# Performance work log

Hardware: AMD Instinct MI355X
Metric: run time of the kernel (lower is better)

The kernel has to match this reference:

```python
import jax, jax.numpy as jnp
import numpy as np

B, Q, K, H = 32, 256, 256, 128

def setup_inputs() -> dict:
    key = jax.random.key(0)
    k1, k2, k3, k4 = jax.random.split(key, 4)
    queries = jax.random.normal(k1, (B, Q, H), dtype=jnp.float32)
    keys = jax.random.normal(k2, (B, K, H), dtype=jnp.float32)
    values = jax.random.normal(k3, (B, K, H), dtype=jnp.float32)
    # nn.Linear(hidden_size, 1, bias=False) weight, stored as a length-H vector
    w = jax.random.normal(k4, (H,), dtype=jnp.float32) * (1.0 / np.sqrt(H))
    return {"queries": queries, "keys": keys, "values": values, "w": w}


def reference(queries, keys, values, w):
    # Y: [B, Q, K, H] broadcast sum, then tanh
    Y = jnp.tanh(queries[:, :, None, :] + keys[:, None, :, :])
    # scores: [B, Q, K] = Y @ w
    scores = jnp.einsum("bqkh,h->bqk", Y, w)
    attn = jax.nn.softmax(scores, axis=-1)
    # output: [B, Q, Hv]
    return jnp.einsum("bqk,bkv->bqv", attn, values)
```

## Files before the change

kernel.cpp:

```cpp
#include <hip/hip_runtime.h>
#include <math.h>

#define C2 2.8853900817779268f

typedef __attribute__((address_space(3))) unsigned int       lds_u32;
typedef const __attribute__((address_space(1))) unsigned int g_u32;

__device__ __forceinline__ void stage16(const float* g, float* l) {
    __builtin_amdgcn_global_load_lds((g_u32*)g, (lds_u32*)l, 16, 0, 0);
}

__global__ __launch_bounds__(512) void addattn_prep(const float* __restrict__ k_g,
                                                    float* __restrict__ ekt)
{
    int tid = blockIdx.x * 512 + threadIdx.x;
    int b   = tid >> 13;
    int r   = tid & 8191;
    int g   = r >> 8;
    int k   = r & 255;
    float4 kv = *(const float4*)(k_g + ((size_t)(b * 256 + k)) * 128 + (g << 2));
    float4 E;
    E.x = __builtin_amdgcn_exp2f(C2 * kv.x);
    E.y = __builtin_amdgcn_exp2f(C2 * kv.y);
    E.z = __builtin_amdgcn_exp2f(C2 * kv.z);
    E.w = __builtin_amdgcn_exp2f(C2 * kv.w);
    *(float4*)(ekt + (size_t)b * 32768 + ((k >> 6) << 13) + (g << 8) + ((k & 63) << 2)) = E;
}

__global__ __launch_bounds__(512) void addattn_kernel(
    const float* __restrict__ q_g, const float* __restrict__ ekt,
    const float* __restrict__ v_g, const float* __restrict__ w_g,
    float* __restrict__ out)
{
    __shared__ float kbuf[32768];
    __shared__ float eqst[4096];
    __shared__ float wlds[128];

    const int tid  = threadIdx.x;
    const int lane = tid & 63;
    const int wv   = __builtin_amdgcn_readfirstlane(tid >> 6);

    const int xcd = blockIdx.x & 7;
    const int sub = blockIdx.x >> 3;
    const int rg  = sub & 7;
    const int b   = (xcd << 2) + (sub >> 3);
    const int qr0 = (rg << 5) + (wv << 2);

    if (tid < 32) ((float4*)wlds)[tid] = ((const float4*)w_g)[tid];

    {
        const float* qb = q_g + (size_t)(b * 256 + qr0) * 128;
        #pragma unroll
        for (int j = 0; j < 2; ++j) {
            int f = lane + (j << 6);
            int r = f >> 5, c = f & 31;
            float4 qv = *(const float4*)(qb + (r << 7) + (c << 2));
            float4 E;
            E.x = __builtin_amdgcn_exp2f(C2 * qv.x);
            E.y = __builtin_amdgcn_exp2f(C2 * qv.y);
            E.z = __builtin_amdgcn_exp2f(C2 * qv.z);
            E.w = __builtin_amdgcn_exp2f(C2 * qv.w);
            *(float4*)&eqst[(wv << 9) + (r << 7) + (c << 2)] = E;
        }
    }

    {
        const float* ekb = ekt + (size_t)b * 32768;
        #pragma unroll
        for (int c = 0; c < 16; ++c) {
            int chunk = (wv << 4) + c;
            stage16(ekb + (chunk << 8) + (lane << 2), kbuf + (chunk << 8));
        }
    }
    __syncthreads();

    const float* eqw = eqst + (wv << 9);
    float s[4][4];
    #pragma unroll
    for (int t = 0; t < 4; ++t)
        #pragma unroll
        for (int r = 0; r < 4; ++r) s[t][r] = 0.f;

    #pragma unroll 2
    for (int g = 0; g < 32; ++g) {
        float4 w4 = *(const float4*)&wlds[g << 2];
        float4 e0 = *(const float4*)&eqw[g << 2];
        float4 e1 = *(const float4*)&eqw[128 + (g << 2)];
        float4 e2 = *(const float4*)&eqw[256 + (g << 2)];
        float4 e3 = *(const float4*)&eqw[384 + (g << 2)];
        #pragma unroll
        for (int t = 0; t < 4; ++t) {
            float4 k4 = *(const float4*)&kbuf[(t << 13) + (g << 8) + (lane << 2)];
            #define RB(E, S)                                                   \
            {                                                                  \
                float d0 = fmaf(E.x, k4.x, 1.f), d1 = fmaf(E.y, k4.y, 1.f);    \
                float d2 = fmaf(E.z, k4.z, 1.f), d3 = fmaf(E.w, k4.w, 1.f);    \
                float P01 = d0 * d1, P23 = d2 * d3;                            \
                float N01 = fmaf(w4.x, d1, w4.y * d0);                         \
                float N23 = fmaf(w4.z, d3, w4.w * d2);                         \
                float num = fmaf(N01, P23, N23 * P01);                         \
                S = fmaf(num, __builtin_amdgcn_rcpf(P01 * P23), S);            \
            }
            RB(e0, s[t][0])
            RB(e1, s[t][1])
            RB(e2, s[t][2])
            RB(e3, s[t][3])
            #undef RB
        }
    }
    __syncthreads();

    float* abase = kbuf + (wv << 10);
    #pragma unroll
    for (int r = 0; r < 4; ++r) {
        float x0 = -C2 * s[0][r], x1 = -C2 * s[1][r];
        float x2 = -C2 * s[2][r], x3 = -C2 * s[3][r];
        float m = fmaxf(fmaxf(x0, x1), fmaxf(x2, x3));
        #pragma unroll
        for (int off = 32; off; off >>= 1) m = fmaxf(m, __shfl_xor(m, off));
        float e0 = __builtin_amdgcn_exp2f(x0 - m);
        float e1 = __builtin_amdgcn_exp2f(x1 - m);
        float e2 = __builtin_amdgcn_exp2f(x2 - m);
        float e3 = __builtin_amdgcn_exp2f(x3 - m);
        float sum = (e0 + e1) + (e2 + e3);
        #pragma unroll
        for (int off = 32; off; off >>= 1) sum += __shfl_xor(sum, off);
        float inv = __builtin_amdgcn_rcpf(sum);
        abase[(r << 8) + lane]       = e0 * inv;
        abase[(r << 8) + 64 + lane]  = e1 * inv;
        abase[(r << 8) + 128 + lane] = e2 * inv;
        abase[(r << 8) + 192 + lane] = e3 * inv;
    }

    float2 o0, o1, o2, o3;
    o0.x = o0.y = o1.x = o1.y = 0.f;
    o2.x = o2.y = o3.x = o3.y = 0.f;
    const float2* vp = (const float2*)(v_g + (size_t)b * 32768) + lane;
    #pragma unroll 4
    for (int j4 = 0; j4 < 64; ++j4) {
        float4 a0 = *(const float4*)(abase + (j4 << 2));
        float4 a1 = *(const float4*)(abase + 256 + (j4 << 2));
        float4 a2 = *(const float4*)(abase + 512 + (j4 << 2));
        float4 a3 = *(const float4*)(abase + 768 + (j4 << 2));
        #pragma unroll
        for (int i = 0; i < 4; ++i) {
            float2 v2 = vp[((j4 << 2) + i) << 6];
            float c0 = (&a0.x)[i], c1 = (&a1.x)[i], c2 = (&a2.x)[i], c3 = (&a3.x)[i];
            o0.x = fmaf(c0, v2.x, o0.x); o0.y = fmaf(c0, v2.y, o0.y);
            o1.x = fmaf(c1, v2.x, o1.x); o1.y = fmaf(c1, v2.y, o1.y);
            o2.x = fmaf(c2, v2.x, o2.x); o2.y = fmaf(c2, v2.y, o2.y);
            o3.x = fmaf(c3, v2.x, o3.x); o3.y = fmaf(c3, v2.y, o3.y);
        }
    }

    float* ob = out + (size_t)(b * 256 + qr0) * 128 + (lane << 1);
    *(float2*)(ob)       = o0;
    *(float2*)(ob + 128) = o1;
    *(float2*)(ob + 256) = o2;
    *(float2*)(ob + 384) = o3;
}

extern "C" void kernel_launch(void* const* d_in, const int* in_sizes, int n_in,
                              void* d_out, int out_size, void* d_ws, size_t ws_size,
                              hipStream_t stream) {
    const float* q = (const float*)d_in[0];
    const float* k = (const float*)d_in[1];
    const float* v = (const float*)d_in[2];
    const float* w = (const float*)d_in[3];
    float* out = (float*)d_out;
    float* ekt = (float*)d_ws;
    addattn_prep<<<512, 512, 0, stream>>>(k, ekt);
    addattn_kernel<<<256, 512, 0, stream>>>(q, ekt, v, w, out);
}
```

Baseline: 49.80 us.

## Double block size to 1024 threads with two query rows per wave

Each block now runs 16 waves instead of 8, and each wave handles 2 query rows instead of 4. The grid stays the same, so per-CU wave parallelism doubles while per-thread work and registers halve. The per-wave query exponentials, the w copy and the attention weights now share one private LDS strip, which removes the second barrier before the softmax write. The cost is more redundant work per block (w copies, more K-stage issue) and fewer rows over which each K load from LDS is reused.

```diff
diff --git a/kernel.cpp b/kernel.cpp
--- a/kernel.cpp
+++ b/kernel.cpp
@@ -27,14 +27,13 @@
     *(float4*)(ekt + (size_t)b * 32768 + ((k >> 6) << 13) + (g << 8) + ((k & 63) << 2)) = E;
 }
 
-__global__ __launch_bounds__(512) void addattn_kernel(
+__global__ __launch_bounds__(1024, 4) void addattn_kernel(
     const float* __restrict__ q_g, const float* __restrict__ ekt,
     const float* __restrict__ v_g, const float* __restrict__ w_g,
     float* __restrict__ out)
 {
     __shared__ float kbuf[32768];
-    __shared__ float eqst[4096];
-    __shared__ float wlds[128];
+    __shared__ float sB[8192];
 
     const int tid  = threadIdx.x;
     const int lane = tid & 63;
@@ -42,52 +41,43 @@
 
     const int xcd = blockIdx.x & 7;
     const int sub = blockIdx.x >> 3;
-    const int rg  = sub & 7;
     const int b   = (xcd << 2) + (sub >> 3);
-    const int qr0 = (rg << 5) + (wv << 2);
+    const int qr0 = ((sub & 7) << 5) + (wv << 1);
 
-    if (tid < 32) ((float4*)wlds)[tid] = ((const float4*)w_g)[tid];
+    float* strip = sB + (wv << 9);
 
+    if (lane < 32) *(float4*)&strip[256 + (lane << 2)] = ((const float4*)w_g)[lane];
     {
         const float* qb = q_g + (size_t)(b * 256 + qr0) * 128;
-        #pragma unroll
-        for (int j = 0; j < 2; ++j) {
-            int f = lane + (j << 6);
-            int r = f >> 5, c = f & 31;
-            float4 qv = *(const float4*)(qb + (r << 7) + (c << 2));
-            float4 E;
-            E.x = __builtin_amdgcn_exp2f(C2 * qv.x);
-            E.y = __builtin_amdgcn_exp2f(C2 * qv.y);
-            E.z = __builtin_amdgcn_exp2f(C2 * qv.z);
-            E.w = __builtin_amdgcn_exp2f(C2 * qv.w);
-            *(float4*)&eqst[(wv << 9) + (r << 7) + (c << 2)] = E;
-        }
+        int r = lane >> 5, c = lane & 31;
+        float4 qv = *(const float4*)(qb + (r << 7) + (c << 2));
+        float4 E;
+        E.x = __builtin_amdgcn_exp2f(C2 * qv.x);
+        E.y = __builtin_amdgcn_exp2f(C2 * qv.y);
+        E.z = __builtin_amdgcn_exp2f(C2 * qv.z);
+        E.w = __builtin_amdgcn_exp2f(C2 * qv.w);
+        *(float4*)&strip[(r << 7) + (c << 2)] = E;
     }
 
     {
         const float* ekb = ekt + (size_t)b * 32768;
         #pragma unroll
-        for (int c = 0; c < 16; ++c) {
-            int chunk = (wv << 4) + c;
+        for (int c = 0; c < 8; ++c) {
+            int chunk = (wv << 3) + c;
             stage16(ekb + (chunk << 8) + (lane << 2), kbuf + (chunk << 8));
         }
     }
     __syncthreads();
 
-    const float* eqw = eqst + (wv << 9);
-    float s[4][4];
+    float s[4][2];
     #pragma unroll
-    for (int t = 0; t < 4; ++t)
-        #pragma unroll
-        for (int r = 0; r < 4; ++r) s[t][r] = 0.f;
+    for (int t = 0; t < 4; ++t) { s[t][0] = 0.f; s[t][1] = 0.f; }
 
-    #pragma unroll 2
+    #pragma unroll 4
     for (int g = 0; g < 32; ++g) {
-        float4 w4 = *(const float4*)&wlds[g << 2];
-        float4 e0 = *(const float4*)&eqw[g << 2];
-        float4 e1 = *(const float4*)&eqw[128 + (g << 2)];
-        float4 e2 = *(const float4*)&eqw[256 + (g << 2)];
-        float4 e3 = *(const float4*)&eqw[384 + (g << 2)];
+        float4 w4 = *(const float4*)&strip[256 + (g << 2)];
+        float4 e0 = *(const float4*)&strip[g << 2];
+        float4 e1 = *(const float4*)&strip[128 + (g << 2)];
         #pragma unroll
         for (int t = 0; t < 4; ++t) {
             float4 k4 = *(const float4*)&kbuf[(t << 13) + (g << 8) + (lane << 2)];
@@ -103,16 +93,12 @@
             }
             RB(e0, s[t][0])
             RB(e1, s[t][1])
-            RB(e2, s[t][2])
-            RB(e3, s[t][3])
             #undef RB
         }
     }
-    __syncthreads();
 
-    float* abase = kbuf + (wv << 10);
     #pragma unroll
-    for (int r = 0; r < 4; ++r) {
+    for (int r = 0; r < 2; ++r) {
         float x0 = -C2 * s[0][r], x1 = -C2 * s[1][r];
         float x2 = -C2 * s[2][r], x3 = -C2 * s[3][r];
         float m = fmaxf(fmaxf(x0, x1), fmaxf(x2, x3));
@@ -126,38 +112,31 @@
         #pragma unroll
         for (int off = 32; off; off >>= 1) sum += __shfl_xor(sum, off);
         float inv = __builtin_amdgcn_rcpf(sum);
-        abase[(r << 8) + lane]       = e0 * inv;
-        abase[(r << 8) + 64 + lane]  = e1 * inv;
-        abase[(r << 8) + 128 + lane] = e2 * inv;
-        abase[(r << 8) + 192 + lane] = e3 * inv;
+        strip[(r << 8) + lane]       = e0 * inv;
+        strip[(r << 8) + 64 + lane]  = e1 * inv;
+        strip[(r << 8) + 128 + lane] = e2 * inv;
+        strip[(r << 8) + 192 + lane] = e3 * inv;
     }
 
-    float2 o0, o1, o2, o3;
+    float2 o0, o1;
     o0.x = o0.y = o1.x = o1.y = 0.f;
-    o2.x = o2.y = o3.x = o3.y = 0.f;
     const float2* vp = (const float2*)(v_g + (size_t)b * 32768) + lane;
-    #pragma unroll 4
+    #pragma unroll 8
     for (int j4 = 0; j4 < 64; ++j4) {
-        float4 a0 = *(const float4*)(abase + (j4 << 2));
-        float4 a1 = *(const float4*)(abase + 256 + (j4 << 2));
-        float4 a2 = *(const float4*)(abase + 512 + (j4 << 2));
-        float4 a3 = *(const float4*)(abase + 768 + (j4 << 2));
+        float4 a0 = *(const float4*)(strip + (j4 << 2));
+        float4 a1 = *(const float4*)(strip + 256 + (j4 << 2));
         #pragma unroll
         for (int i = 0; i < 4; ++i) {
             float2 v2 = vp[((j4 << 2) + i) << 6];
-            float c0 = (&a0.x)[i], c1 = (&a1.x)[i], c2 = (&a2.x)[i], c3 = (&a3.x)[i];
+            float c0 = (&a0.x)[i], c1 = (&a1.x)[i];
             o0.x = fmaf(c0, v2.x, o0.x); o0.y = fmaf(c0, v2.y, o0.y);
             o1.x = fmaf(c1, v2.x, o1.x); o1.y = fmaf(c1, v2.y, o1.y);
-            o2.x = fmaf(c2, v2.x, o2.x); o2.y = fmaf(c2, v2.y, o2.y);
-            o3.x = fmaf(c3, v2.x, o3.x); o3.y = fmaf(c3, v2.y, o3.y);
         }
     }
 
     float* ob = out + (size_t)(b * 256 + qr0) * 128 + (lane << 1);
     *(float2*)(ob)       = o0;
     *(float2*)(ob + 128) = o1;
-    *(float2*)(ob + 256) = o2;
-    *(float2*)(ob + 384) = o3;
 }
 
 extern "C" void kernel_launch(void* const* d_in, const int* in_sizes, int n_in,
@@ -170,5 +149,5 @@
     float* out = (float*)d_out;
     float* ekt = (float*)d_ws;
     addattn_prep<<<512, 512, 0, stream>>>(k, ekt);
-    addattn_kernel<<<256, 512, 0, stream>>>(q, ekt, v, w, out);
+    addattn_kernel<<<256, 1024, 0, stream>>>(q, ekt, v, w, out);
 }
```

New measurement: 53.01 us. 1.06x slower.
